# Optimization experiments

Measured on AMD Instinct MI355X. Metric: run time of the kernel, lower is better.

## Reference

```python
import jax, jax.numpy as jnp
import numpy as np

D_MODEL = 1024
N_HEADS = 16
LN_EPS = 1e-6  # flax LayerNorm default

def setup_inputs() -> dict:
    key = jax.random.key(0)
    k1, k2, k3 = jax.random.split(key, 3)
    B, S = 2, 2048
    x = jax.random.normal(k1, (B, S, D_MODEL), dtype=jnp.float32)
    W_qkv = jax.random.normal(k2, (D_MODEL, 3 * D_MODEL), dtype=jnp.float32) / np.sqrt(D_MODEL)
    W_out = jax.random.normal(k3, (D_MODEL, D_MODEL), dtype=jnp.float32) / np.sqrt(D_MODEL)
    q_scale = jnp.ones((D_MODEL,), dtype=jnp.float32)
    k_scale = jnp.ones((D_MODEL,), dtype=jnp.float32)
    return {"x": x, "W_qkv": W_qkv, "q_scale": q_scale, "k_scale": k_scale, "W_out": W_out}

def _layernorm(t, scale):
    mu = jnp.mean(t, axis=-1, keepdims=True)
    var = jnp.var(t, axis=-1, keepdims=True)
    return (t - mu) * jax.lax.rsqrt(var + LN_EPS) * scale

def reference(x, W_qkv, q_scale, k_scale, W_out):
    B, S, D = x.shape
    H = N_HEADS
    Hd = D // H
    # fused QKV projection (no bias)
    qkv = jnp.einsum('bsd,de->bse', x, W_qkv)
    q, k, v = jnp.split(qkv, 3, axis=-1)
    # QK-LayerNorm over full d_model (before head split), scale only
    q = _layernorm(q, q_scale)
    k = _layernorm(k, k_scale)
    # split heads: [b, s, h, hd]
    q = q.reshape(B, S, H, Hd)
    k = k.reshape(B, S, H, Hd)
    v = v.reshape(B, S, H, Hd)
    # eager attention with causal mask
    scores = jnp.einsum('bshd,bthd->bhst', q / jnp.sqrt(Hd).astype(q.dtype), k)  # [b,h,s,t]
    future = jnp.triu(jnp.ones((S, S), dtype=bool), 1)  # True on strictly-future positions
    scores = jnp.where(future[None, None, :, :], jnp.finfo(scores.dtype).min, scores)
    attn = jax.nn.softmax(scores, axis=-1)
    ctx = jnp.einsum('bhst,bthd->bshd', attn, v)
    out = jnp.einsum('bsd,de->bse', ctx.reshape(B, S, D), W_out)
    return out
```

## Files before the change

### kernel.cpp

```cpp
#include <hip/hip_runtime.h>
#include <cstdint>
#include <cstddef>

typedef __attribute__((ext_vector_type(8))) short short8;
typedef __attribute__((ext_vector_type(4))) float floatx4;

__device__ __forceinline__ float bf2f(unsigned short u) {
  union { unsigned int i; float f; } c; c.i = ((unsigned int)u) << 16; return c.f;
}
__device__ __forceinline__ unsigned short f2bf(float f) {
  union { float f; unsigned int i; } c; c.f = f;
  unsigned int r = c.i + 0x7fffu + ((c.i >> 16) & 1u);
  return (unsigned short)(r >> 16);
}
__device__ __forceinline__ unsigned int fbits(float f) {
  union { float f; unsigned int i; } c; c.f = f; return c.i;
}

__device__ __forceinline__ void glds16(const unsigned short* g, unsigned short* l) {
  __builtin_amdgcn_global_load_lds((const __attribute__((address_space(1))) void*)g,
                                   (__attribute__((address_space(3))) void*)l, 16, 0, 0);
}

__device__ __forceinline__ void tr_tile(const float* __restrict__ in,
                                        unsigned short* __restrict__ out,
                                        int R, int C, int bx, int by, int tid,
                                        unsigned short (*t)[33]) {
  const int cx = tid & 31, rl = tid >> 5;
#pragma unroll
  for (int i = 0; i < 4; ++i)
    t[rl + i * 8][cx] = f2bf(in[(size_t)(by * 32 + rl + i * 8) * C + bx * 32 + cx]);
  __syncthreads();
  const int oc = by * 32 + cx;
#pragma unroll
  for (int i = 0; i < 4; ++i)
    out[(size_t)(bx * 32 + rl + i * 8) * R + oc] = t[cx][rl + i * 8];
}

__global__ __launch_bounds__(256) void k_prep(const float* __restrict__ x,
                                              const float* __restrict__ Wq,
                                              const float* __restrict__ Wo,
                                              unsigned short* __restrict__ x_bf,
                                              unsigned short* __restrict__ WTq,
                                              unsigned short* __restrict__ WTo) {
  __shared__ unsigned short t[32][33];
  const int bid = blockIdx.x, tid = threadIdx.x;
  if (bid < 3072) {
    tr_tile(Wq, WTq, 1024, 3072, bid % 96, bid / 96, tid, t);
  } else if (bid < 4096) {
    int v = bid - 3072;
    tr_tile(Wo, WTo, 1024, 1024, v & 31, v >> 5, tid, t);
  } else {
    int i = (bid - 4096) * 256 + tid;
    float4 v = ((const float4*)x)[i];
    ushort4 o = { f2bf(v.x), f2bf(v.y), f2bf(v.z), f2bf(v.w) };
    ((ushort4*)x_bf)[i] = o;
  }
}

template <int MT, bool F32OUT>
__global__ __launch_bounds__(256) void k_gemm_bt(const unsigned short* __restrict__ A,
                                                 const unsigned short* __restrict__ BT,
                                                 void* __restrict__ Cout,
                                                 int M, int N, int K) {
  constexpr int NI = MT / 32;
  __shared__ unsigned short As[2][MT * 32];
  __shared__ unsigned short Bs[2][128 * 32];
  const int bm = blockIdx.x * MT, bn = blockIdx.y * 128;
  const int tid = threadIdx.x;
  const int wave = tid >> 6, lane = tid & 63;
  const int wm = (wave & 1) * (MT / 2), wn = (wave >> 1) * 64;
  const int lrow = lane & 15, lgrp = lane >> 4;
  floatx4 acc[NI][4] = {};

  const int lr4 = lane >> 2, lc8 = (lane & 3) * 8;
  const int br0 = wave * 32;
  const unsigned short* Bg0 = BT + (size_t)(bn + br0 + lr4) * K + lc8;
  const unsigned short* Bg1 = BT + (size_t)(bn + br0 + 16 + lr4) * K + lc8;
  const int ar0 = wave * (MT / 4);
  const unsigned short* Ag0 = A + (size_t)(bm + ar0 + lr4) * K + lc8;
  const unsigned short* Ag1 = A + (size_t)(bm + ar0 + 16 + lr4) * K + lc8;

  for (int k0 = 0; k0 < K; k0 += 64) {
#pragma unroll
    for (int u = 0; u < 2; ++u) {
      const int ko = k0 + u * 32;
      glds16(Ag0 + ko, &As[u][ar0 * 32]);
      if (MT == 128) glds16(Ag1 + ko, &As[u][(ar0 + 16) * 32]);
      glds16(Bg0 + ko, &Bs[u][br0 * 32]);
      glds16(Bg1 + ko, &Bs[u][(br0 + 16) * 32]);
    }
    __syncthreads();
#pragma unroll
    for (int u = 0; u < 2; ++u) {
      short8 a[NI], bfr[4];
#pragma unroll
      for (int i = 0; i < NI; ++i)
        a[i] = *(const short8*)&As[u][(wm + i * 16 + lrow) * 32 + lgrp * 8];
#pragma unroll
      for (int j = 0; j < 4; ++j)
        bfr[j] = *(const short8*)&Bs[u][(wn + j * 16 + lrow) * 32 + lgrp * 8];
#pragma unroll
      for (int i = 0; i < NI; ++i)
#pragma unroll
        for (int j = 0; j < 4; ++j)
          acc[i][j] = __builtin_amdgcn_mfma_f32_16x16x32_bf16(a[i], bfr[j], acc[i][j], 0, 0, 0);
    }
    __syncthreads();
  }
#pragma unroll
  for (int i = 0; i < NI; ++i)
#pragma unroll
    for (int j = 0; j < 4; ++j)
#pragma unroll
      for (int r = 0; r < 4; ++r) {
        int m = bm + wm + i * 16 + lgrp * 4 + r;
        int n = bn + wn + j * 16 + lrow;
        if (F32OUT)
          ((float*)Cout)[(size_t)m * N + n] = acc[i][j][r];
        else
          ((unsigned short*)Cout)[(size_t)m * N + n] = f2bf(acc[i][j][r]);
      }
}

__global__ __launch_bounds__(256) void k_lnv(const unsigned short* __restrict__ qkv,
                                             const float* __restrict__ q_scale,
                                             const float* __restrict__ k_scale,
                                             unsigned short* __restrict__ q_n,
                                             unsigned short* __restrict__ k_n,
                                             unsigned short* __restrict__ VT) {
  const int bid = blockIdx.x, tid = threadIdx.x;
  if (bid < 4096) {
    const int tok = bid;
    const int wave = tid >> 6, lane = tid & 63;
    __shared__ float red[2][4];
    const unsigned short* row = qkv + (size_t)tok * 3072;
#pragma unroll
    for (int seg = 0; seg < 2; ++seg) {
      const unsigned short* p  = row + seg * 1024;
      const float* sc = seg ? k_scale : q_scale;
      unsigned short* outp = (seg ? k_n : q_n) + (size_t)tok * 1024;
      ushort4 u = *(const ushort4*)&p[tid * 4];
      float xv[4] = { bf2f(u.x), bf2f(u.y), bf2f(u.z), bf2f(u.w) };
      float sum = xv[0] + xv[1] + xv[2] + xv[3];
      float sq  = xv[0]*xv[0] + xv[1]*xv[1] + xv[2]*xv[2] + xv[3]*xv[3];
      for (int off = 32; off; off >>= 1) {
        sum += __shfl_down(sum, off, 64);
        sq  += __shfl_down(sq,  off, 64);
      }
      if (lane == 0) { red[0][wave] = sum; red[1][wave] = sq; }
      __syncthreads();
      sum = red[0][0] + red[0][1] + red[0][2] + red[0][3];
      sq  = red[1][0] + red[1][1] + red[1][2] + red[1][3];
      __syncthreads();
      float mean = sum * (1.0f / 1024.0f);
      float var  = sq * (1.0f / 1024.0f) - mean * mean;
      float rstd = rsqrtf(var + 1e-6f);
      if (seg == 0) rstd *= 0.18033688011112042f;
      float4 su = *(const float4*)&sc[tid * 4];
      ushort4 o;
      o.x = f2bf((xv[0] - mean) * rstd * su.x);
      o.y = f2bf((xv[1] - mean) * rstd * su.y);
      o.z = f2bf((xv[2] - mean) * rstd * su.z);
      o.w = f2bf((xv[3] - mean) * rstd * su.w);
      *(ushort4*)&outp[tid * 4] = o;
    }
  } else {
    __shared__ unsigned short t[32][33];
    const int v = bid - 4096;
    const int bh = v & 31, b = bh >> 4, h = bh & 15;
    const int sy = (v >> 5) & 63, hx = v >> 11;
    const int cx = tid & 31, rl = tid >> 5;
#pragma unroll
    for (int i = 0; i < 4; ++i)
      t[rl + i * 8][cx] =
        qkv[(size_t)(b * 2048 + sy * 32 + rl + i * 8) * 3072 + 2048 + h * 64 + hx * 32 + cx];
    __syncthreads();
#pragma unroll
    for (int i = 0; i < 4; ++i)
      VT[((size_t)bh * 64 + hx * 32 + rl + i * 8) * 2048 + sy * 32 + cx] = t[cx][rl + i * 8];
  }
}


#define KS_STRIDE 72
#define VS_STRIDE 136
#define PS_STRIDE 136

template <bool MASKED>
__device__ __forceinline__ void attn_step(int t0, int q0, int wq, int wt,
    const short8 (&qa)[2][2],
    const unsigned short* Ks, const unsigned short* Vs, unsigned short* Psq,
    floatx4 (&o)[2][4], float (&l)[2], int lrow, int lgrp) {
  const int twbase = wt * 64;
#pragma unroll
  for (int tb = 0; tb < 4; ++tb) {
    short8 kb0 = *(const short8*)&Ks[(twbase + tb * 16 + lrow) * KS_STRIDE + lgrp * 8];
    short8 kb1 = *(const short8*)&Ks[(twbase + tb * 16 + lrow) * KS_STRIDE + 32 + lgrp * 8];
#pragma unroll
    for (int qb = 0; qb < 2; ++qb) {
      floatx4 st = {};
      st = __builtin_amdgcn_mfma_f32_16x16x32_bf16(kb0, qa[qb][0], st, 0, 0, 0);
      st = __builtin_amdgcn_mfma_f32_16x16x32_bf16(kb1, qa[qb][1], st, 0, 0, 0);
      float p0 = exp2f(st[0]), p1 = exp2f(st[1]);
      float p2 = exp2f(st[2]), p3 = exp2f(st[3]);
      if (MASKED) {
        const int qcol = q0 + wq * 32 + qb * 16 + lrow;
        const int tbase = t0 + twbase + tb * 16 + lgrp * 4;
        p0 = (tbase     <= qcol) ? p0 : 0.0f;
        p1 = (tbase + 1 <= qcol) ? p1 : 0.0f;
        p2 = (tbase + 2 <= qcol) ? p2 : 0.0f;
        p3 = (tbase + 3 <= qcol) ? p3 : 0.0f;
      }
      l[qb] += (p0 + p1) + (p2 + p3);
      uint2 pu;
      pu.x = (fbits(p0) >> 16) | (fbits(p1) & 0xFFFF0000u);
      pu.y = (fbits(p2) >> 16) | (fbits(p3) & 0xFFFF0000u);
      *(uint2*)&Psq[(qb * 16 + lrow) * PS_STRIDE + twbase + tb * 16 + lgrp * 4] = pu;
    }
  }
#pragma unroll
  for (int kk = 0; kk < 2; ++kk) {
    short8 pa0 = *(const short8*)&Psq[lrow * PS_STRIDE + twbase + kk * 32 + lgrp * 8];
    short8 pa1 = *(const short8*)&Psq[(16 + lrow) * PS_STRIDE + twbase + kk * 32 + lgrp * 8];
#pragma unroll
    for (int hb = 0; hb < 4; ++hb) {
      short8 vb = *(const short8*)&Vs[(hb * 16 + lrow) * VS_STRIDE + twbase + kk * 32 + lgrp * 8];
      o[0][hb] = __builtin_amdgcn_mfma_f32_16x16x32_bf16(pa0, vb, o[0][hb], 0, 0, 0);
      o[1][hb] = __builtin_amdgcn_mfma_f32_16x16x32_bf16(pa1, vb, o[1][hb], 0, 0, 0);
    }
  }
}

__global__ __launch_bounds__(256) void k_flash(const unsigned short* __restrict__ q_n,
                                               const unsigned short* __restrict__ k_n,
                                               const unsigned short* __restrict__ VT,
                                               unsigned short* __restrict__ ctx) {
  const int S = 2048, D = 1024;
  const int bh = blockIdx.x, b = bh >> 4, h = bh & 15;
  const int qt = 31 - (int)blockIdx.y;
  const int q0 = qt * 64;
  const int tid = threadIdx.x, wave = tid >> 6, lane = tid & 63;
  const int wq = wave >> 1, wt = wave & 1;
  const int lrow = lane & 15, lgrp = lane >> 4;

  __shared__ __align__(16) unsigned char smem[53248];
  unsigned short* Ks  = (unsigned short*)smem;
  unsigned short* Vs  = (unsigned short*)(smem + 18432);
  unsigned short* Psq = (unsigned short*)(smem + 35840) + wq * 32 * PS_STRIDE;
  float* buf  = (float*)smem;
  float* Lbuf = (float*)(smem + 17408);

  const unsigned short* kg = k_n + (size_t)(b * S) * D + h * 64;
  const unsigned short* vg = VT + (size_t)bh * 64 * S;
  const int ksr = tid >> 3, ksc = (tid & 7) * 8;
  const int vsr = tid >> 4, vsc = (tid & 15) * 8;

  short8 qa[2][2];
#pragma unroll
  for (int qb = 0; qb < 2; ++qb) {
    const unsigned short* qp =
        q_n + (size_t)(b * S + q0 + wq * 32 + qb * 16 + lrow) * D + h * 64;
    qa[qb][0] = *(const short8*)(qp + lgrp * 8);
    qa[qb][1] = *(const short8*)(qp + 32 + lgrp * 8);
  }
  floatx4 o[2][4] = {};
  float l[2] = {};

  const int tend = q0 + 64;
  for (int t0 = 0; t0 < tend; t0 += 128) {
#pragma unroll
    for (int j = 0; j < 4; ++j) {
      int r = ksr + j * 32;
      *(int4*)&Ks[r * KS_STRIDE + ksc] = *(const int4*)(kg + (size_t)(t0 + r) * D + ksc);
    }
#pragma unroll
    for (int j = 0; j < 4; ++j) {
      int r = vsr + j * 16;
      *(int4*)&Vs[r * VS_STRIDE + vsc] = *(const int4*)(vg + (size_t)r * S + t0 + vsc);
    }
    __syncthreads();
    const bool half = (tend - t0) < 128;
    if (!(half && wt == 1)) {
      if (t0 + 128 <= q0)
        attn_step<false>(t0, q0, wq, wt, qa, Ks, Vs, Psq, o, l, lrow, lgrp);
      else
        attn_step<true>(t0, q0, wq, wt, qa, Ks, Vs, Psq, o, l, lrow, lgrp);
    }
    __syncthreads();
  }

#pragma unroll
  for (int qb = 0; qb < 2; ++qb) {
    l[qb] += __shfl_xor(l[qb], 16, 64);
    l[qb] += __shfl_xor(l[qb], 32, 64);
  }
  if (wt == 1) {
    if (lane < 16) {
      Lbuf[wq * 32 + lrow]      = l[0];
      Lbuf[wq * 32 + 16 + lrow] = l[1];
    }
    float* bf = buf + wq * 32 * 68;
#pragma unroll
    for (int qb = 0; qb < 2; ++qb)
#pragma unroll
      for (int hb = 0; hb < 4; ++hb)
#pragma unroll
        for (int r = 0; r < 4; ++r)
          bf[(qb * 16 + lgrp * 4 + r) * 68 + hb * 16 + lrow] = o[qb][hb][r];
  }
  __syncthreads();
  if (wt == 0) {
    float* bf = buf + wq * 32 * 68;
#pragma unroll
    for (int qb = 0; qb < 2; ++qb) {
      l[qb] += Lbuf[wq * 32 + qb * 16 + lrow];
#pragma unroll
      for (int hb = 0; hb < 4; ++hb)
#pragma unroll
        for (int r = 0; r < 4; ++r)
          o[qb][hb][r] += bf[(qb * 16 + lgrp * 4 + r) * 68 + hb * 16 + lrow];
    }
    unsigned short* op = ctx + (size_t)(b * S + q0 + wq * 32) * D + h * 64;
#pragma unroll
    for (int qb = 0; qb < 2; ++qb)
#pragma unroll
      for (int r = 0; r < 4; ++r) {
        float inv = 1.0f / __shfl(l[qb], lgrp * 4 + r, 64);
        int row = qb * 16 + lgrp * 4 + r;
#pragma unroll
        for (int hb = 0; hb < 4; ++hb)
          op[(size_t)row * D + hb * 16 + lrow] = f2bf(o[qb][hb][r] * inv);
      }
  }
}

extern "C" void kernel_launch(void* const* d_in, const int* in_sizes, int n_in,
                              void* d_out, int out_size, void* d_ws, size_t ws_size,
                              hipStream_t stream) {
  const float* x       = (const float*)d_in[0];
  const float* W_qkv   = (const float*)d_in[1];
  const float* q_scale = (const float*)d_in[2];
  const float* k_scale = (const float*)d_in[3];
  const float* W_out   = (const float*)d_in[4];
  float* out = (float*)d_out;
  char* ws = (char*)d_ws;
  unsigned short* WT_qkv = (unsigned short*)(ws + 0);
  unsigned short* WT_out = (unsigned short*)(ws + 6291456);
  unsigned short* qkv    = (unsigned short*)(ws + 8388608);
  unsigned short* q_nb   = (unsigned short*)(ws + 33554432);
  unsigned short* k_nb   = (unsigned short*)(ws + 41943040);
  unsigned short* VT     = (unsigned short*)(ws + 50331648);
  unsigned short* x_bf   = (unsigned short*)(ws + 58720256);
  unsigned short* ctx    = qkv;

  k_prep<<<8192, 256, 0, stream>>>(x, W_qkv, W_out, x_bf, WT_qkv, WT_out);
  k_gemm_bt<128, false><<<dim3(32, 24), 256, 0, stream>>>(x_bf, WT_qkv, qkv, 4096, 3072, 1024);
  k_lnv<<<8192, 256, 0, stream>>>(qkv, q_scale, k_scale, q_nb, k_nb, VT);
  k_flash<<<dim3(32, 32), 256, 0, stream>>>(q_nb, k_nb, VT, ctx);
  k_gemm_bt<64, true><<<dim3(64, 8), 256, 0, stream>>>(ctx, WT_out, out, 4096, 1024, 1024);
}
```

Baseline: 183.8 us.

## Load K and V fragments directly from global memory instead of staging through LDS

The flash-attention kernel no longer stages K and V tiles in shared memory. Each wave now reads its MFMA operands straight from global memory (L2/L1), which removes two __syncthreads per iteration and shrinks LDS use so more blocks can be resident (launch_bounds now requests 4). The fp32-to-bf16 packing also switches to a single byte-permute instruction. The cost is more global/cache traffic, since K/V are no longer shared across waves, and global-load latency now sits directly in front of the MFMAs.

After: 237.4 us. 29.2% more time.

```diff
diff --git a/kernel.cpp b/kernel.cpp
--- a/kernel.cpp
+++ b/kernel.cpp
@@ -183,20 +183,21 @@
 }
 
 
-#define KS_STRIDE 72
-#define VS_STRIDE 136
 #define PS_STRIDE 136
 
 template <bool MASKED>
 __device__ __forceinline__ void attn_step(int t0, int q0, int wq, int wt,
     const short8 (&qa)[2][2],
-    const unsigned short* Ks, const unsigned short* Vs, unsigned short* Psq,
+    const unsigned short* __restrict__ kg,
+    const unsigned short* __restrict__ vg,
+    unsigned short* Psq,
     floatx4 (&o)[2][4], float (&l)[2], int lrow, int lgrp) {
   const int twbase = wt * 64;
 #pragma unroll
   for (int tb = 0; tb < 4; ++tb) {
-    short8 kb0 = *(const short8*)&Ks[(twbase + tb * 16 + lrow) * KS_STRIDE + lgrp * 8];
-    short8 kb1 = *(const short8*)&Ks[(twbase + tb * 16 + lrow) * KS_STRIDE + 32 + lgrp * 8];
+    const unsigned short* kp = kg + (size_t)(t0 + twbase + tb * 16 + lrow) * 1024 + lgrp * 8;
+    short8 kb0 = *(const short8*)kp;
+    short8 kb1 = *(const short8*)(kp + 32);
 #pragma unroll
     for (int qb = 0; qb < 2; ++qb) {
       floatx4 st = {};
@@ -214,8 +215,8 @@
       }
       l[qb] += (p0 + p1) + (p2 + p3);
       uint2 pu;
-      pu.x = (fbits(p0) >> 16) | (fbits(p1) & 0xFFFF0000u);
-      pu.y = (fbits(p2) >> 16) | (fbits(p3) & 0xFFFF0000u);
+      pu.x = __builtin_amdgcn_perm(fbits(p1), fbits(p0), 0x07060302u);
+      pu.y = __builtin_amdgcn_perm(fbits(p3), fbits(p2), 0x07060302u);
       *(uint2*)&Psq[(qb * 16 + lrow) * PS_STRIDE + twbase + tb * 16 + lgrp * 4] = pu;
     }
   }
@@ -225,17 +226,18 @@
     short8 pa1 = *(const short8*)&Psq[(16 + lrow) * PS_STRIDE + twbase + kk * 32 + lgrp * 8];
 #pragma unroll
     for (int hb = 0; hb < 4; ++hb) {
-      short8 vb = *(const short8*)&Vs[(hb * 16 + lrow) * VS_STRIDE + twbase + kk * 32 + lgrp * 8];
+      short8 vb = *(const short8*)(vg + (size_t)(hb * 16 + lrow) * 2048
+                                   + t0 + twbase + kk * 32 + lgrp * 8);
       o[0][hb] = __builtin_amdgcn_mfma_f32_16x16x32_bf16(pa0, vb, o[0][hb], 0, 0, 0);
       o[1][hb] = __builtin_amdgcn_mfma_f32_16x16x32_bf16(pa1, vb, o[1][hb], 0, 0, 0);
     }
   }
 }
 
-__global__ __launch_bounds__(256) void k_flash(const unsigned short* __restrict__ q_n,
-                                               const unsigned short* __restrict__ k_n,
-                                               const unsigned short* __restrict__ VT,
-                                               unsigned short* __restrict__ ctx) {
+__global__ __launch_bounds__(256, 4) void k_flash(const unsigned short* __restrict__ q_n,
+                                                  const unsigned short* __restrict__ k_n,
+                                                  const unsigned short* __restrict__ VT,
+                                                  unsigned short* __restrict__ ctx) {
   const int S = 2048, D = 1024;
   const int bh = blockIdx.x, b = bh >> 4, h = bh & 15;
   const int qt = 31 - (int)blockIdx.y;
@@ -244,17 +246,13 @@
   const int wq = wave >> 1, wt = wave & 1;
   const int lrow = lane & 15, lgrp = lane >> 4;
 
-  __shared__ __align__(16) unsigned char smem[53248];
-  unsigned short* Ks  = (unsigned short*)smem;
-  unsigned short* Vs  = (unsigned short*)(smem + 18432);
-  unsigned short* Psq = (unsigned short*)(smem + 35840) + wq * 32 * PS_STRIDE;
+  __shared__ __align__(16) unsigned char smem[17664];
+  unsigned short* Psq = (unsigned short*)smem + wq * 32 * PS_STRIDE;
   float* buf  = (float*)smem;
   float* Lbuf = (float*)(smem + 17408);
 
   const unsigned short* kg = k_n + (size_t)(b * S) * D + h * 64;
   const unsigned short* vg = VT + (size_t)bh * 64 * S;
-  const int ksr = tid >> 3, ksc = (tid & 7) * 8;
-  const int vsr = tid >> 4, vsc = (tid & 15) * 8;
 
   short8 qa[2][2];
 #pragma unroll
@@ -269,26 +267,15 @@
 
   const int tend = q0 + 64;
   for (int t0 = 0; t0 < tend; t0 += 128) {
-#pragma unroll
-    for (int j = 0; j < 4; ++j) {
-      int r = ksr + j * 32;
-      *(int4*)&Ks[r * KS_STRIDE + ksc] = *(const int4*)(kg + (size_t)(t0 + r) * D + ksc);
-    }
-#pragma unroll
-    for (int j = 0; j < 4; ++j) {
-      int r = vsr + j * 16;
-      *(int4*)&Vs[r * VS_STRIDE + vsc] = *(const int4*)(vg + (size_t)r * S + t0 + vsc);
-    }
-    __syncthreads();
     const bool half = (tend - t0) < 128;
     if (!(half && wt == 1)) {
       if (t0 + 128 <= q0)
-        attn_step<false>(t0, q0, wq, wt, qa, Ks, Vs, Psq, o, l, lrow, lgrp);
+        attn_step<false>(t0, q0, wq, wt, qa, kg, vg, Psq, o, l, lrow, lgrp);
       else
-        attn_step<true>(t0, q0, wq, wt, qa, Ks, Vs, Psq, o, l, lrow, lgrp);
-    }
-    __syncthreads();
-  }
+        attn_step<true>(t0, q0, wq, wt, qa, kg, vg, Psq, o, l, lrow, lgrp);
+    }
+  }
+  __syncthreads();
 
 #pragma unroll
   for (int qb = 0; qb < 2; ++qb) {
```
